# Optimization experiments

Measured on AMD Instinct MI355X. Metric: run time of the kernel, lower is better.

Reference implementation:

```python
import jax, jax.numpy as jnp
import numpy as np

N = 100000   # nodes
E = 1200000  # edges
IN, HID, OUT = 64, 64, 64
G = 64       # graphs in the batch


def setup_inputs() -> dict:
    key = jax.random.key(0)
    ks = jax.random.split(key, 7)
    x = jax.random.normal(ks[0], (N, IN), dtype=jnp.float32)
    edge_index = jax.random.randint(ks[1], (2, E), 0, N, dtype=jnp.int32)
    batch = jnp.sort(jax.random.randint(ks[2], (N,), 0, G, dtype=jnp.int32))
    W1 = jax.random.normal(ks[3], (IN, HID), dtype=jnp.float32) * (1.0 / np.sqrt(IN))
    b1 = jnp.zeros((HID,), dtype=jnp.float32)
    W2 = jax.random.normal(ks[4], (HID, OUT), dtype=jnp.float32) * (1.0 / np.sqrt(HID))
    b2 = jnp.zeros((OUT,), dtype=jnp.float32)
    return {"x": x, "edge_index": edge_index, "batch": batch,
            "W1": W1, "b1": b1, "W2": W2, "b2": b2}


def _gcn_conv(x, W, b, src, dst, dinv):
    # x' = D^{-1/2} (A + I) D^{-1/2} (x W) + b   (PyG GCNConv with self-loops)
    h = x @ W                                   # [N, F_out]
    norm = dinv[src] * dinv[dst]                # [E]
    agg = jax.ops.segment_sum(h[src] * norm[:, None], dst, num_segments=N)
    agg = agg + h * (dinv * dinv)[:, None]      # self-loop contribution
    return agg + b


def reference(x, edge_index, batch, W1, b1, W2, b2):
    src, dst = edge_index[0], edge_index[1]
    # degree with self-loops, counted at the aggregation target (PyG convention)
    deg = jax.ops.segment_sum(jnp.ones((E,), x.dtype), dst, num_segments=N) + 1.0
    dinv = jax.lax.rsqrt(deg)

    h1 = jax.nn.relu(_gcn_conv(x, W1, b1, src, dst, dinv))   # [N, HID]
    s1 = jax.ops.segment_sum(h1, batch, num_segments=G)      # [G, HID]
    h2 = jax.nn.relu(_gcn_conv(h1, W2, b2, src, dst, dinv))  # [N, OUT]
    s2 = jax.ops.segment_sum(h2, batch, num_segments=G)      # [G, OUT]
    return h2, jnp.concatenate([s1, s2], axis=1)
```

## Files before the change

### kernel.cpp

```cpp
#include <hip/hip_runtime.h>


#define FDIM 64
#define BSHIFT 7
#define MAXNB 1024
#define EBCAP 2048
#define COLCAP 3072
#define BCAP 4096

__device__ __forceinline__ unsigned short f2bf(float f) {
    union { float f; unsigned int u; } a; a.f = f;
    unsigned int u = a.u;
    unsigned int r = u + 0x7fffu + ((u >> 16) & 1u);
    return (unsigned short)(r >> 16);
}
__device__ __forceinline__ float bf2f(unsigned short s) {
    union { unsigned int u; float f; } a; a.u = ((unsigned int)s) << 16;
    return a.f;
}

__global__ __launch_bounds__(256, 4) void k_pre(
    const int* __restrict__ src, const int* __restrict__ dstp, int E,
    int N, int gemmB,
    const float* __restrict__ x, const float* __restrict__ W1,
    int* __restrict__ bucketFill,
    unsigned short* __restrict__ gb1, unsigned int* __restrict__ ebuf) {
    __shared__ __align__(16) char sm[33792];
    int tid = threadIdx.x;
    int bx = blockIdx.x;
    if (bx < gemmB) {
        float4* Ws = (float4*)sm;
        float (*Xs)[68] = (float(*)[68])(sm + 16384);
        ushort4* GB4 = (ushort4*)gb1;
        if (bx == 0 && tid < 16) GB4[(size_t)N * 16 + tid] = make_ushort4(0, 0, 0, 0);
        const float4* W4 = (const float4*)W1;
        for (int i = tid; i < 1024; i += 256) Ws[i] = W4[i];
        int rowBase = bx * 64;
        for (int i = tid; i < 1024; i += 256) {
            int r = i >> 4, f4 = i & 15;
            float4 v = make_float4(0.f, 0.f, 0.f, 0.f);
            if (rowBase + r < N) v = ((const float4*)x)[(size_t)(rowBase + r) * 16 + f4];
            *(float4*)&Xs[r][f4 * 4] = v;
        }
        __syncthreads();
        int r0 = (tid >> 4) * 4;
        int c4 = tid & 15;
        float4 acc0 = make_float4(0,0,0,0), acc1 = acc0, acc2 = acc0, acc3 = acc0;
#pragma unroll 16
        for (int k = 0; k < 64; k++) {
            float4 w = Ws[k * 16 + c4];
            float x0 = Xs[r0 + 0][k], x1 = Xs[r0 + 1][k], x2 = Xs[r0 + 2][k], x3 = Xs[r0 + 3][k];
            acc0.x += x0 * w.x; acc0.y += x0 * w.y; acc0.z += x0 * w.z; acc0.w += x0 * w.w;
            acc1.x += x1 * w.x; acc1.y += x1 * w.y; acc1.z += x1 * w.z; acc1.w += x1 * w.w;
            acc2.x += x2 * w.x; acc2.y += x2 * w.y; acc2.z += x2 * w.z; acc2.w += x2 * w.w;
            acc3.x += x3 * w.x; acc3.y += x3 * w.y; acc3.z += x3 * w.z; acc3.w += x3 * w.w;
        }
        float4 a[4] = {acc0, acc1, acc2, acc3};
#pragma unroll
        for (int i = 0; i < 4; i++) {
            int row = rowBase + r0 + i;
            if (row < N) {
                ushort4 pk;
                pk.x = f2bf(a[i].x); pk.y = f2bf(a[i].y);
                pk.z = f2bf(a[i].z); pk.w = f2bf(a[i].w);
                GB4[(size_t)row * 16 + c4] = pk;
            }
        }
        return;
    }
    int* hist = (int*)sm;
    int* base = hist + MAXNB;
    for (int i = tid; i < MAXNB; i += 256) hist[i] = 0;
    __syncthreads();
    int e0 = (bx - gemmB) * 4096;
    int s[16], d[16], r[16];
#pragma unroll
    for (int k = 0; k < 16; k++) {
        int e = e0 + k * 256 + tid;
        bool valid = e < E;
        s[k] = valid ? src[e] : 0;
        d[k] = valid ? dstp[e] : 0;
        r[k] = valid ? atomicAdd(&hist[d[k] >> BSHIFT], 1) : 0;
    }
    __syncthreads();
    for (int i = tid; i < MAXNB; i += 256) {
        int c = hist[i];
        base[i] = c ? (i << 11) + atomicAdd(&bucketFill[i], c) : 0;
    }
    __syncthreads();
#pragma unroll
    for (int k = 0; k < 16; k++) {
        int e = e0 + k * 256 + tid;
        if (e < E)
            ebuf[base[d[k] >> BSHIFT] + r[k]] =
                (unsigned int)s[k] | ((unsigned int)(d[k] & 127) << 17);
    }
}

__global__ __launch_bounds__(256) void k_bsort(const unsigned int* __restrict__ ebuf,
                                               const int* __restrict__ bucketFill, int N,
                                               int* __restrict__ row_ptr,
                                               int* __restrict__ row_blocks,
                                               int* __restrict__ col,
                                               float* __restrict__ dinv,
                                               float* __restrict__ pool, int poolLen) {
    __shared__ int cntL[128];
    __shared__ int scanL[128];
    __shared__ int fillL[128];
    __shared__ int colL[BCAP];
    __shared__ int padT;
    int b = blockIdx.x;
    int n0 = b << BSHIFT;
    int nCnt = N - n0; if (nCnt > 128) nCnt = 128;
    int t = threadIdx.x;
    if (b == 0 && t == 0) dinv[N] = 0.f;
    if (b == 0) {
        for (int i = t; i < poolLen; i += 256) pool[i] = 0.f;
    }
    int cnt = bucketFill[b]; if (cnt > EBCAP) cnt = EBCAP;
    int lo = b << 11, hi = lo + cnt;
    int outBase = b * COLCAP;
    if (t < 128) { cntL[t] = 0; fillL[t] = 0; }
    __syncthreads();
    for (int e = lo + t; e < hi; e += 256)
        atomicAdd(&cntL[ebuf[e] >> 17], 1);
    __syncthreads();
    int pc = 0;
    if (t < 128) { pc = (cntL[t] + 7) & ~7; scanL[t] = pc; }
    __syncthreads();
    for (int off = 1; off < 128; off <<= 1) {
        int u = (t >= off && t < 128) ? scanL[t - off] : 0;
        __syncthreads();
        if (t < 128) scanL[t] += u;
        __syncthreads();
    }
    if (t == 127) padT = scanL[127];
    if (t < nCnt) {
        int ex = scanL[t] - pc;
        row_ptr[n0 + t] = outBase + ex;
        row_blocks[n0 + t] = pc >> 3;
        dinv[n0 + t] = rsqrtf((float)cntL[t] + 1.0f);
        scanL[t] = ex;
    }
    __syncthreads();
    int padTotal = padT;
    if (padTotal <= BCAP) {
        for (int i = t; i < padTotal; i += 256) colL[i] = N;
        __syncthreads();
        for (int e = lo + t; e < hi; e += 256) {
            unsigned int pr = ebuf[e];
            int d = pr >> 17;
            int r = scanL[d] + atomicAdd(&fillL[d], 1);
            colL[r] = (int)(pr & 0x1FFFFu);
        }
        __syncthreads();
        for (int i = t; i < padTotal; i += 256) col[outBase + i] = colL[i];
    } else {
        for (int e = lo + t; e < hi; e += 256) {
            unsigned int pr = ebuf[e];
            int d = pr >> 17;
            int r = scanL[d] + atomicAdd(&fillL[d], 1);
            col[outBase + r] = (int)(pr & 0x1FFFFu);
        }
        __syncthreads();
        if (t < nCnt) {
            int pcl = (cntL[t] + 7) & ~7;
            for (int i = cntL[t]; i < pcl; i++) col[outBase + scanL[t] + i] = N;
        }
    }
}

template <typename OutT, bool EDGE_DINV>
__global__ __launch_bounds__(256) void k_agg(
    const unsigned short* __restrict__ Gb,
    const int* __restrict__ row_ptr, const int* __restrict__ row_blocks,
    const int* __restrict__ col, const float* __restrict__ dinv,
    const float* __restrict__ bias, int N, OutT* __restrict__ Out) {
    int w = threadIdx.x >> 6;
    int c = threadIdx.x & 63;
    int n = blockIdx.x * 4 + w;
    if (n >= N) return;
    int e = row_ptr[n];
    int nb8 = row_blocks[n];
    float dn = dinv[n];
    float self = bf2f(Gb[(size_t)n * FDIM + c]);
    float acc = EDGE_DINV ? self * dn : self;
    for (; nb8 >= 2; nb8 -= 2, e += 16) {
        int4 ca = *(const int4*)(col + e);
        int4 cb = *(const int4*)(col + e + 4);
        int4 cc = *(const int4*)(col + e + 8);
        int4 cd = *(const int4*)(col + e + 12);
        int s0  = __builtin_amdgcn_readfirstlane(ca.x);
        int s1  = __builtin_amdgcn_readfirstlane(ca.y);
        int s2  = __builtin_amdgcn_readfirstlane(ca.z);
        int s3  = __builtin_amdgcn_readfirstlane(ca.w);
        int s4  = __builtin_amdgcn_readfirstlane(cb.x);
        int s5  = __builtin_amdgcn_readfirstlane(cb.y);
        int s6  = __builtin_amdgcn_readfirstlane(cb.z);
        int s7  = __builtin_amdgcn_readfirstlane(cb.w);
        int s8  = __builtin_amdgcn_readfirstlane(cc.x);
        int s9  = __builtin_amdgcn_readfirstlane(cc.y);
        int s10 = __builtin_amdgcn_readfirstlane(cc.z);
        int s11 = __builtin_amdgcn_readfirstlane(cc.w);
        int s12 = __builtin_amdgcn_readfirstlane(cd.x);
        int s13 = __builtin_amdgcn_readfirstlane(cd.y);
        int s14 = __builtin_amdgcn_readfirstlane(cd.z);
        int s15 = __builtin_amdgcn_readfirstlane(cd.w);
        float a0  = bf2f(Gb[(size_t)s0  * FDIM + c]);
        float a1  = bf2f(Gb[(size_t)s1  * FDIM + c]);
        float a2  = bf2f(Gb[(size_t)s2  * FDIM + c]);
        float a3  = bf2f(Gb[(size_t)s3  * FDIM + c]);
        float a4  = bf2f(Gb[(size_t)s4  * FDIM + c]);
        float a5  = bf2f(Gb[(size_t)s5  * FDIM + c]);
        float a6  = bf2f(Gb[(size_t)s6  * FDIM + c]);
        float a7  = bf2f(Gb[(size_t)s7  * FDIM + c]);
        float a8  = bf2f(Gb[(size_t)s8  * FDIM + c]);
        float a9  = bf2f(Gb[(size_t)s9  * FDIM + c]);
        float a10 = bf2f(Gb[(size_t)s10 * FDIM + c]);
        float a11 = bf2f(Gb[(size_t)s11 * FDIM + c]);
        float a12 = bf2f(Gb[(size_t)s12 * FDIM + c]);
        float a13 = bf2f(Gb[(size_t)s13 * FDIM + c]);
        float a14 = bf2f(Gb[(size_t)s14 * FDIM + c]);
        float a15 = bf2f(Gb[(size_t)s15 * FDIM + c]);
        if constexpr (EDGE_DINV) {
            float d0  = dinv[s0],  d1  = dinv[s1],  d2  = dinv[s2],  d3  = dinv[s3];
            float d4  = dinv[s4],  d5  = dinv[s5],  d6  = dinv[s6],  d7  = dinv[s7];
            float d8  = dinv[s8],  d9  = dinv[s9],  d10 = dinv[s10], d11 = dinv[s11];
            float d12 = dinv[s12], d13 = dinv[s13], d14 = dinv[s14], d15 = dinv[s15];
            acc += (((a0*d0 + a1*d1) + (a2*d2 + a3*d3)) + ((a4*d4 + a5*d5) + (a6*d6 + a7*d7)))
                 + (((a8*d8 + a9*d9) + (a10*d10 + a11*d11)) + ((a12*d12 + a13*d13) + (a14*d14 + a15*d15)));
        } else {
            acc += (((a0 + a1) + (a2 + a3)) + ((a4 + a5) + (a6 + a7)))
                 + (((a8 + a9) + (a10 + a11)) + ((a12 + a13) + (a14 + a15)));
        }
    }
    if (nb8) {
        int4 ca = *(const int4*)(col + e);
        int4 cb = *(const int4*)(col + e + 4);
        int s0 = __builtin_amdgcn_readfirstlane(ca.x);
        int s1 = __builtin_amdgcn_readfirstlane(ca.y);
        int s2 = __builtin_amdgcn_readfirstlane(ca.z);
        int s3 = __builtin_amdgcn_readfirstlane(ca.w);
        int s4 = __builtin_amdgcn_readfirstlane(cb.x);
        int s5 = __builtin_amdgcn_readfirstlane(cb.y);
        int s6 = __builtin_amdgcn_readfirstlane(cb.z);
        int s7 = __builtin_amdgcn_readfirstlane(cb.w);
        float a0 = bf2f(Gb[(size_t)s0 * FDIM + c]);
        float a1 = bf2f(Gb[(size_t)s1 * FDIM + c]);
        float a2 = bf2f(Gb[(size_t)s2 * FDIM + c]);
        float a3 = bf2f(Gb[(size_t)s3 * FDIM + c]);
        float a4 = bf2f(Gb[(size_t)s4 * FDIM + c]);
        float a5 = bf2f(Gb[(size_t)s5 * FDIM + c]);
        float a6 = bf2f(Gb[(size_t)s6 * FDIM + c]);
        float a7 = bf2f(Gb[(size_t)s7 * FDIM + c]);
        if constexpr (EDGE_DINV) {
            float d0 = dinv[s0], d1 = dinv[s1], d2 = dinv[s2], d3 = dinv[s3];
            float d4 = dinv[s4], d5 = dinv[s5], d6 = dinv[s6], d7 = dinv[s7];
            acc += ((a0*d0 + a1*d1) + (a2*d2 + a3*d3)) + ((a4*d4 + a5*d5) + (a6*d6 + a7*d7));
        } else {
            acc += ((a0 + a1) + (a2 + a3)) + ((a4 + a5) + (a6 + a7));
        }
    }
    float v = fmaxf(acc * dn + bias[c], 0.f);
    if constexpr (sizeof(OutT) == 2)
        Out[(size_t)n * FDIM + c] = f2bf(v);
    else
        Out[(size_t)n * FDIM + c] = v;
}

__global__ __launch_bounds__(256, 4) void k_gemm2(
    const unsigned short* __restrict__ H1b, const float* __restrict__ W2,
    const float* __restrict__ dinv, const int* __restrict__ batch, int N,
    unsigned short* __restrict__ Gb2, float* __restrict__ pool) {
    __shared__ float4 Ws[64 * 16];
    __shared__ float Xs[64][68];
    __shared__ int bsL[64];
    int tid = threadIdx.x;
    ushort4* GB4 = (ushort4*)Gb2;
    if (blockIdx.x == 0 && tid < 16)
        GB4[(size_t)N * 16 + tid] = make_ushort4(0, 0, 0, 0);
    const float4* W4 = (const float4*)W2;
    for (int i = tid; i < 1024; i += 256) Ws[i] = W4[i];
    int rowBase = blockIdx.x * 64;
    if (tid < 64) {
        int row = rowBase + tid;
        bsL[tid] = (row < N) ? batch[row] : -1;
    }
    const ushort4* H4 = (const ushort4*)H1b;
    for (int i = tid; i < 1024; i += 256) {
        int r = i >> 4, u4 = i & 15;
        float4 v = make_float4(0.f, 0.f, 0.f, 0.f);
        if (rowBase + r < N) {
            ushort4 u = H4[(size_t)(rowBase + r) * 16 + u4];
            v = make_float4(bf2f(u.x), bf2f(u.y), bf2f(u.z), bf2f(u.w));
        }
        *(float4*)&Xs[r][u4 * 4] = v;
    }
    __syncthreads();
    int r0 = (tid >> 4) * 4;
    int c4 = tid & 15;
    float4 acc0 = make_float4(0,0,0,0), acc1 = acc0, acc2 = acc0, acc3 = acc0;
#pragma unroll 16
    for (int k = 0; k < 64; k++) {
        float4 w = Ws[k * 16 + c4];
        float x0 = Xs[r0 + 0][k], x1 = Xs[r0 + 1][k], x2 = Xs[r0 + 2][k], x3 = Xs[r0 + 3][k];
        acc0.x += x0 * w.x; acc0.y += x0 * w.y; acc0.z += x0 * w.z; acc0.w += x0 * w.w;
        acc1.x += x1 * w.x; acc1.y += x1 * w.y; acc1.z += x1 * w.z; acc1.w += x1 * w.w;
        acc2.x += x2 * w.x; acc2.y += x2 * w.y; acc2.z += x2 * w.z; acc2.w += x2 * w.w;
        acc3.x += x3 * w.x; acc3.y += x3 * w.y; acc3.z += x3 * w.z; acc3.w += x3 * w.w;
    }
    float4 a[4] = {acc0, acc1, acc2, acc3};
#pragma unroll
    for (int i = 0; i < 4; i++) {
        int row = rowBase + r0 + i;
        if (row < N) {
            float dn = dinv[row];
            ushort4 pk;
            pk.x = f2bf(a[i].x * dn);
            pk.y = f2bf(a[i].y * dn);
            pk.z = f2bf(a[i].z * dn);
            pk.w = f2bf(a[i].w * dn);
            GB4[(size_t)row * 16 + c4] = pk;
        }
    }
    {
        int cc = tid & 63;
        int seg = tid >> 6;
        float run = 0.f; int gcur = -2;
        for (int rl = 0; rl < 16; rl++) {
            int r = seg * 16 + rl;
            int g = bsL[r];
            if (g < 0) break;
            if (g != gcur) {
                if (gcur >= 0) atomicAdd(&pool[(size_t)gcur * 128 + cc], run);
                run = 0.f; gcur = g;
            }
            run += Xs[r][cc];
        }
        if (gcur >= 0) atomicAdd(&pool[(size_t)gcur * 128 + cc], run);
    }
}

__global__ __launch_bounds__(256) void k_pool2(const float* __restrict__ H2,
                                               const int* __restrict__ batch,
                                               int N, float* __restrict__ pool) {
    int w = threadIdx.x >> 6;
    int c = threadIdx.x & 63;
    int r0 = blockIdx.x * 256 + w * 64;
    int rEnd = r0 + 64; if (rEnd > N) rEnd = N;
    float run = 0.f; int gcur = -2;
    int r = r0;
    for (; r + 8 <= rEnd; r += 8) {
        float v0 = H2[(size_t)(r + 0) * FDIM + c];
        float v1 = H2[(size_t)(r + 1) * FDIM + c];
        float v2 = H2[(size_t)(r + 2) * FDIM + c];
        float v3 = H2[(size_t)(r + 3) * FDIM + c];
        float v4 = H2[(size_t)(r + 4) * FDIM + c];
        float v5 = H2[(size_t)(r + 5) * FDIM + c];
        float v6 = H2[(size_t)(r + 6) * FDIM + c];
        float v7 = H2[(size_t)(r + 7) * FDIM + c];
        float vv[8] = {v0, v1, v2, v3, v4, v5, v6, v7};
#pragma unroll
        for (int k = 0; k < 8; k++) {
            int g = __builtin_amdgcn_readfirstlane(batch[r + k]);
            if (g != gcur) {
                if (gcur >= 0) atomicAdd(&pool[(size_t)gcur * 128 + 64 + c], run);
                run = 0.f; gcur = g;
            }
            run += vv[k];
        }
    }
    for (; r < rEnd; r++) {
        int g = __builtin_amdgcn_readfirstlane(batch[r]);
        if (g != gcur) {
            if (gcur >= 0) atomicAdd(&pool[(size_t)gcur * 128 + 64 + c], run);
            run = 0.f; gcur = g;
        }
        run += H2[(size_t)r * FDIM + c];
    }
    if (gcur >= 0) atomicAdd(&pool[(size_t)gcur * 128 + 64 + c], run);
}

static inline size_t align256(size_t x) { return (x + 255) & ~(size_t)255; }

extern "C" void kernel_launch(void* const* d_in, const int* in_sizes, int n_in,
                              void* d_out, int out_size, void* d_ws, size_t ws_size,
                              hipStream_t stream) {
    const float* x     = (const float*)d_in[0];
    const int*   ei    = (const int*)d_in[1];
    const int*   batch = (const int*)d_in[2];
    const float* W1    = (const float*)d_in[3];
    const float* b1    = (const float*)d_in[4];
    const float* W2    = (const float*)d_in[5];
    const float* b2    = (const float*)d_in[6];

    const int N = in_sizes[0] / FDIM;
    const int E = in_sizes[1] / 2;
    const int G = 64;
    const int NB = (N + 127) >> BSHIFT;
    const int* src = ei;
    const int* dst = ei + E;

    char* p = (char*)d_ws;
    int* row_ptr     = (int*)p; p += align256(((size_t)N + 1) * 4);
    int* row_blocks  = (int*)p; p += align256((size_t)N * 4);
    int* col         = (int*)p; p += align256((size_t)NB * COLCAP * 4);
    int* bucketFill  = (int*)p; p += align256((size_t)MAXNB * 4);
    float* dinv      = (float*)p; p += align256(((size_t)N + 1) * 4);
    unsigned short* gb1 = (unsigned short*)p; p += align256(((size_t)N + 1) * FDIM * 2);
    unsigned short* gb2 = (unsigned short*)p; p += align256(((size_t)N + 1) * FDIM * 2);
    unsigned short* h1b = (unsigned short*)p; p += align256((size_t)N * FDIM * 2);
    unsigned int* ebuf = (unsigned int*)h1b;

    float* out  = (float*)d_out;
    float* h2   = out;
    float* pool = out + (size_t)N * FDIM;

    hipMemsetAsync(bucketFill, 0, (size_t)MAXNB * 4, stream);

    int gemmB = (N + 63) / 64;
    int aggB  = (N + 3) / 4;
    int scatB = (E + 4095) / 4096;
    int poolB = (N + 255) / 256;

    k_pre<<<gemmB + scatB, 256, 0, stream>>>(src, dst, E, N, gemmB, x, W1,
                                             bucketFill, gb1, ebuf);
    k_bsort<<<NB, 256, 0, stream>>>(ebuf, bucketFill, N, row_ptr, row_blocks,
                                    col, dinv, pool, G * 128);
    k_agg<unsigned short, true><<<aggB, 256, 0, stream>>>(
        gb1, row_ptr, row_blocks, col, dinv, b1, N, h1b);
    k_gemm2<<<gemmB, 256, 0, stream>>>(h1b, W2, dinv, batch, N, gb2, pool);
    k_agg<float, false><<<aggB, 256, 0, stream>>>(
        gb2, row_ptr, row_blocks, col, dinv, b2, N, h2);
    k_pool2<<<poolB, 256, 0, stream>>>(h2, batch, N, pool);
}
```

Measured before the change: 232.4 us.

## Fuse second-layer GEMM into first aggregation and merge both pooling passes

The separate k_gemm2 kernel is removed. Each wave now computes h1·W2 right after producing its h1 row in the first aggregation, broadcasting the 64 values with shuffles and reading W2 from shared memory. The first-layer pooling moves into the final pooling kernel, which now reads both the bf16 h1 and the fp32 h2 rows. This drops one launch and one full read of h1. The cost is 64 serial shuffle-FMA steps per node in the aggregation kernel, plus 16KB of dynamic shared memory per block that may reduce occupancy.

```diff
diff --git a/kernel.cpp b/kernel.cpp
--- a/kernel.cpp
+++ b/kernel.cpp
@@ -103,7 +103,8 @@
                                                int* __restrict__ row_blocks,
                                                int* __restrict__ col,
                                                float* __restrict__ dinv,
-                                               float* __restrict__ pool, int poolLen) {
+                                               float* __restrict__ pool, int poolLen,
+                                               unsigned short* __restrict__ gb2) {
     __shared__ int cntL[128];
     __shared__ int scanL[128];
     __shared__ int fillL[128];
@@ -116,6 +117,7 @@
     if (b == 0 && t == 0) dinv[N] = 0.f;
     if (b == 0) {
         for (int i = t; i < poolLen; i += 256) pool[i] = 0.f;
+        if (t < 16) ((ushort4*)gb2)[(size_t)N * 16 + t] = make_ushort4(0, 0, 0, 0);
     }
     int cnt = bucketFill[b]; if (cnt > EBCAP) cnt = EBCAP;
     int lo = b << 11, hi = lo + cnt;
@@ -170,12 +172,20 @@
     }
 }
 
-template <typename OutT, bool EDGE_DINV>
+template <typename OutT, bool EDGE_DINV, bool MATVEC>
 __global__ __launch_bounds__(256) void k_agg(
     const unsigned short* __restrict__ Gb,
     const int* __restrict__ row_ptr, const int* __restrict__ row_blocks,
     const int* __restrict__ col, const float* __restrict__ dinv,
-    const float* __restrict__ bias, int N, OutT* __restrict__ Out) {
+    const float* __restrict__ bias, int N, OutT* __restrict__ Out,
+    const float* __restrict__ W2mat, unsigned short* __restrict__ Gb2out) {
+    extern __shared__ float Ws[];
+    if constexpr (MATVEC) {
+        float4* W4s = (float4*)Ws;
+        const float4* W4 = (const float4*)W2mat;
+        for (int i = threadIdx.x; i < 1024; i += 256) W4s[i] = W4[i];
+        __syncthreads();
+    }
     int w = threadIdx.x >> 6;
     int c = threadIdx.x & 63;
     int n = blockIdx.x * 4 + w;
@@ -266,91 +276,36 @@
         Out[(size_t)n * FDIM + c] = f2bf(v);
     else
         Out[(size_t)n * FDIM + c] = v;
-}
-
-__global__ __launch_bounds__(256, 4) void k_gemm2(
-    const unsigned short* __restrict__ H1b, const float* __restrict__ W2,
-    const float* __restrict__ dinv, const int* __restrict__ batch, int N,
-    unsigned short* __restrict__ Gb2, float* __restrict__ pool) {
-    __shared__ float4 Ws[64 * 16];
-    __shared__ float Xs[64][68];
-    __shared__ int bsL[64];
-    int tid = threadIdx.x;
-    ushort4* GB4 = (ushort4*)Gb2;
-    if (blockIdx.x == 0 && tid < 16)
-        GB4[(size_t)N * 16 + tid] = make_ushort4(0, 0, 0, 0);
-    const float4* W4 = (const float4*)W2;
-    for (int i = tid; i < 1024; i += 256) Ws[i] = W4[i];
-    int rowBase = blockIdx.x * 64;
-    if (tid < 64) {
-        int row = rowBase + tid;
-        bsL[tid] = (row < N) ? batch[row] : -1;
-    }
-    const ushort4* H4 = (const ushort4*)H1b;
-    for (int i = tid; i < 1024; i += 256) {
-        int r = i >> 4, u4 = i & 15;
-        float4 v = make_float4(0.f, 0.f, 0.f, 0.f);
-        if (rowBase + r < N) {
-            ushort4 u = H4[(size_t)(rowBase + r) * 16 + u4];
-            v = make_float4(bf2f(u.x), bf2f(u.y), bf2f(u.z), bf2f(u.w));
-        }
-        *(float4*)&Xs[r][u4 * 4] = v;
-    }
-    __syncthreads();
-    int r0 = (tid >> 4) * 4;
-    int c4 = tid & 15;
-    float4 acc0 = make_float4(0,0,0,0), acc1 = acc0, acc2 = acc0, acc3 = acc0;
-#pragma unroll 16
-    for (int k = 0; k < 64; k++) {
-        float4 w = Ws[k * 16 + c4];
-        float x0 = Xs[r0 + 0][k], x1 = Xs[r0 + 1][k], x2 = Xs[r0 + 2][k], x3 = Xs[r0 + 3][k];
-        acc0.x += x0 * w.x; acc0.y += x0 * w.y; acc0.z += x0 * w.z; acc0.w += x0 * w.w;
-        acc1.x += x1 * w.x; acc1.y += x1 * w.y; acc1.z += x1 * w.z; acc1.w += x1 * w.w;
-        acc2.x += x2 * w.x; acc2.y += x2 * w.y; acc2.z += x2 * w.z; acc2.w += x2 * w.w;
-        acc3.x += x3 * w.x; acc3.y += x3 * w.y; acc3.z += x3 * w.z; acc3.w += x3 * w.w;
-    }
-    float4 a[4] = {acc0, acc1, acc2, acc3};
+    if constexpr (MATVEC) {
+        float sum = 0.f;
 #pragma unroll
-    for (int i = 0; i < 4; i++) {
-        int row = rowBase + r0 + i;
-        if (row < N) {
-            float dn = dinv[row];
-            ushort4 pk;
-            pk.x = f2bf(a[i].x * dn);
-            pk.y = f2bf(a[i].y * dn);
-            pk.z = f2bf(a[i].z * dn);
-            pk.w = f2bf(a[i].w * dn);
-            GB4[(size_t)row * 16 + c4] = pk;
-        }
-    }
-    {
-        int cc = tid & 63;
-        int seg = tid >> 6;
-        float run = 0.f; int gcur = -2;
-        for (int rl = 0; rl < 16; rl++) {
-            int r = seg * 16 + rl;
-            int g = bsL[r];
-            if (g < 0) break;
-            if (g != gcur) {
-                if (gcur >= 0) atomicAdd(&pool[(size_t)gcur * 128 + cc], run);
-                run = 0.f; gcur = g;
-            }
-            run += Xs[r][cc];
-        }
-        if (gcur >= 0) atomicAdd(&pool[(size_t)gcur * 128 + cc], run);
-    }
-}
-
-__global__ __launch_bounds__(256) void k_pool2(const float* __restrict__ H2,
-                                               const int* __restrict__ batch,
-                                               int N, float* __restrict__ pool) {
+        for (int c2 = 0; c2 < 64; c2++) {
+            float vc = __shfl(v, c2);
+            sum += vc * Ws[c2 * 64 + c];
+        }
+        Gb2out[(size_t)n * FDIM + c] = f2bf(dn * sum);
+    }
+}
+
+__global__ __launch_bounds__(256) void k_pool12(const unsigned short* __restrict__ H1b,
+                                                const float* __restrict__ H2,
+                                                const int* __restrict__ batch,
+                                                int N, float* __restrict__ pool) {
     int w = threadIdx.x >> 6;
     int c = threadIdx.x & 63;
     int r0 = blockIdx.x * 256 + w * 64;
     int rEnd = r0 + 64; if (rEnd > N) rEnd = N;
-    float run = 0.f; int gcur = -2;
+    float run1 = 0.f, run2 = 0.f; int gcur = -2;
     int r = r0;
     for (; r + 8 <= rEnd; r += 8) {
+        float u0 = bf2f(H1b[(size_t)(r + 0) * FDIM + c]);
+        float u1 = bf2f(H1b[(size_t)(r + 1) * FDIM + c]);
+        float u2 = bf2f(H1b[(size_t)(r + 2) * FDIM + c]);
+        float u3 = bf2f(H1b[(size_t)(r + 3) * FDIM + c]);
+        float u4 = bf2f(H1b[(size_t)(r + 4) * FDIM + c]);
+        float u5 = bf2f(H1b[(size_t)(r + 5) * FDIM + c]);
+        float u6 = bf2f(H1b[(size_t)(r + 6) * FDIM + c]);
+        float u7 = bf2f(H1b[(size_t)(r + 7) * FDIM + c]);
         float v0 = H2[(size_t)(r + 0) * FDIM + c];
         float v1 = H2[(size_t)(r + 1) * FDIM + c];
         float v2 = H2[(size_t)(r + 2) * FDIM + c];
@@ -359,26 +314,38 @@
         float v5 = H2[(size_t)(r + 5) * FDIM + c];
         float v6 = H2[(size_t)(r + 6) * FDIM + c];
         float v7 = H2[(size_t)(r + 7) * FDIM + c];
+        float uu[8] = {u0, u1, u2, u3, u4, u5, u6, u7};
         float vv[8] = {v0, v1, v2, v3, v4, v5, v6, v7};
 #pragma unroll
         for (int k = 0; k < 8; k++) {
             int g = __builtin_amdgcn_readfirstlane(batch[r + k]);
             if (g != gcur) {
-                if (gcur >= 0) atomicAdd(&pool[(size_t)gcur * 128 + 64 + c], run);
-                run = 0.f; gcur = g;
+                if (gcur >= 0) {
+                    atomicAdd(&pool[(size_t)gcur * 128 + c], run1);
+                    atomicAdd(&pool[(size_t)gcur * 128 + 64 + c], run2);
+                }
+                run1 = 0.f; run2 = 0.f; gcur = g;
             }
-            run += vv[k];
+            run1 += uu[k];
+            run2 += vv[k];
         }
     }
     for (; r < rEnd; r++) {
         int g = __builtin_amdgcn_readfirstlane(batch[r]);
         if (g != gcur) {
-            if (gcur >= 0) atomicAdd(&pool[(size_t)gcur * 128 + 64 + c], run);
-            run = 0.f; gcur = g;
-        }
-        run += H2[(size_t)r * FDIM + c];
-    }
-    if (gcur >= 0) atomicAdd(&pool[(size_t)gcur * 128 + 64 + c], run);
+            if (gcur >= 0) {
+                atomicAdd(&pool[(size_t)gcur * 128 + c], run1);
+                atomicAdd(&pool[(size_t)gcur * 128 + 64 + c], run2);
+            }
+            run1 = 0.f; run2 = 0.f; gcur = g;
+        }
+        run1 += bf2f(H1b[(size_t)r * FDIM + c]);
+        run2 += H2[(size_t)r * FDIM + c];
+    }
+    if (gcur >= 0) {
+        atomicAdd(&pool[(size_t)gcur * 128 + c], run1);
+        atomicAdd(&pool[(size_t)gcur * 128 + 64 + c], run2);
+    }
 }
 
 static inline size_t align256(size_t x) { return (x + 255) & ~(size_t)255; }
@@ -426,11 +393,10 @@
     k_pre<<<gemmB + scatB, 256, 0, stream>>>(src, dst, E, N, gemmB, x, W1,
                                              bucketFill, gb1, ebuf);
     k_bsort<<<NB, 256, 0, stream>>>(ebuf, bucketFill, N, row_ptr, row_blocks,
-                                    col, dinv, pool, G * 128);
-    k_agg<unsigned short, true><<<aggB, 256, 0, stream>>>(
-        gb1, row_ptr, row_blocks, col, dinv, b1, N, h1b);
-    k_gemm2<<<gemmB, 256, 0, stream>>>(h1b, W2, dinv, batch, N, gb2, pool);
-    k_agg<float, false><<<aggB, 256, 0, stream>>>(
-        gb2, row_ptr, row_blocks, col, dinv, b2, N, h2);
-    k_pool2<<<poolB, 256, 0, stream>>>(h2, batch, N, pool);
-}
+                                    col, dinv, pool, G * 128, gb2);
+    k_agg<unsigned short, true, true><<<aggB, 256, 16384, stream>>>(
+        gb1, row_ptr, row_blocks, col, dinv, b1, N, h1b, W2, gb2);
+    k_agg<float, false, false><<<aggB, 256, 0, stream>>>(
+        gb2, row_ptr, row_blocks, col, dinv, b2, N, h2, nullptr, nullptr);
+    k_pool12<<<poolB, 256, 0, stream>>>(h1b, h2, batch, N, pool);
+}
```

Measured after the change: 278.0 us. +19.7%, slower.
